# Optimization experiments

Hardware: AMD Instinct MI355X
Metric: run time of the kernel (lower is better)

The kernel has to match this reference:

```python
import jax, jax.numpy as jnp
import numpy as np

B, N = 256, 256
EPS = 1e-5

def _bn_per_sample(x, g, b):
    # Torch code applies BatchNorm1d(C) to each sample (N, C) independently in
    # training mode -> normalize over the node axis per channel, per sample.
    m = jnp.mean(x, axis=1, keepdims=True)
    v = jnp.mean((x - m) ** 2, axis=1, keepdims=True)  # biased var, as BN uses
    return (x - m) * jax.lax.rsqrt(v + EPS) * g + b

def _mpl(adj, x, W):
    # message passing: aggregate over dense adjacency then project + ReLU
    agg = jnp.einsum('nm,bmd->bnd', adj, x)
    return jnp.maximum(agg @ W, 0.0)

def _green(adj, x, W):
    # GreenBlock: concat input with MPL output -> doubles channel dim
    return jnp.concatenate([x, _mpl(adj, x, W)], axis=-1)

def setup_inputs() -> dict:
    key = jax.random.key(0)
    ks = jax.random.split(key, 16)
    def w(k, shape):
        fan_in = shape[0]
        return jax.random.normal(k, shape, jnp.float32) / np.sqrt(fan_in)
    return {
        'x': jax.random.normal(ks[0], (B, N, 1), jnp.float32),
        'adj': jax.random.uniform(ks[1], (N, N), jnp.float32),
        'W_fst': w(ks[2], (1, 64)),
        'W_snd': w(ks[3], (64, 64)),
        'W_thrd': w(ks[4], (128, 128)),
        'W_thrdb': w(ks[5], (256, 256)),
        'W_frth': w(ks[6], (256, 256)),
        'W_ffth': w(ks[7], (320, 256)),
        'bn6_g': jnp.ones((256,), jnp.float32), 'bn6_b': jnp.zeros((256,), jnp.float32),
        'W_svth': w(ks[8], (256, 256)),
        'bn8_g': jnp.ones((512,), jnp.float32), 'bn8_b': jnp.zeros((512,), jnp.float32),
        'W_nnth': w(ks[9], (512, 512)),
        'W_tnth': w(ks[10], (1024, 1024)),
        'W_lvnth': w(ks[11], (1280, 256)),
        'bn12_g': jnp.ones((256,), jnp.float32), 'bn12_b': jnp.zeros((256,), jnp.float32),
        'W_ff1': w(ks[12], (576, 128)), 'b_ff1': jnp.zeros((128,), jnp.float32),
        'W_ff2': w(ks[13], (128, 1)), 'b_ff2': jnp.zeros((1,), jnp.float32),
        'W_final': w(ks[14], (1, 1)),
    }

def reference(x, adj, W_fst, W_snd, W_thrd, W_thrdb, W_frth, W_ffth,
              bn6_g, bn6_b, W_svth, bn8_g, bn8_b, W_nnth, W_tnth, W_lvnth,
              bn12_g, bn12_b, W_ff1, b_ff1, W_ff2, b_ff2, W_final):
    b, n = x.shape[0], x.shape[1]
    skip_1 = x @ W_fst                                   # (B,N,64)
    skip_2 = _green(adj, skip_1, W_snd)                  # (B,N,128)
    skip_2 = _green(adj, skip_2, W_thrd)                 # (B,N,256)
    skip_2 = _mpl(adj, skip_2, W_thrdb)                  # (B,N,256)
    skip_2 = _mpl(adj, skip_2, W_frth)                   # (B,N,256)
    skip_2 = jnp.concatenate([skip_1, skip_2], axis=2)   # (B,N,320)
    skip_2 = skip_2 @ W_ffth                             # (B,N,256)
    skip_2 = _bn_per_sample(skip_2, bn6_g, bn6_b)
    skip_3 = _green(adj, skip_2, W_svth)                 # (B,N,512)
    skip_3 = _bn_per_sample(skip_3, bn8_g, bn8_b)
    skip_3 = _green(adj, skip_3, W_nnth)                 # (B,N,1024)
    skip_3 = _mpl(adj, skip_3, W_tnth)                   # (B,N,1024)
    skip_3 = jnp.concatenate([skip_3, skip_2], axis=2)   # (B,N,1280)
    skip_3 = skip_3 @ W_lvnth                            # (B,N,256)
    skip_3 = _bn_per_sample(skip_3, bn12_g, bn12_b)
    last = jnp.concatenate([skip_3, skip_2, skip_1], axis=2)  # (B,N,576)
    last = jnp.maximum(last @ W_ff1 + b_ff1, 0.0) @ W_ff2 + b_ff2  # (B,N,1)
    last = (last @ W_final).reshape(b, n)
    return jax.nn.softmax(last, axis=-1)
```

## Files before the change

### kernel.cpp

```cpp
#include <hip/hip_runtime.h>
#include <math.h>

#define NBATCH 256
#define NNODE 256
#define FCLAMP 60000.0f

typedef float f32x4 __attribute__((ext_vector_type(4)));
typedef _Float16 half_t;
typedef half_t f16x8 __attribute__((ext_vector_type(8)));
typedef half_t f16x4 __attribute__((ext_vector_type(4)));

__device__ __forceinline__ void split2(float v, half_t& h, half_t& l)
{
    v = fminf(fmaxf(v, -FCLAMP), FCLAMP);
    half_t hh = (half_t)v;
    h = hh;
    l = (half_t)(v - (float)hh);
}

template<bool RELU, bool ACC>
__global__ __launch_bounds__(256)
void gemm_wk2(int M, int N, int K,
              const float* __restrict__ A, int lda,
              const half_t* __restrict__ Bh, const half_t* __restrict__ Bl, int ldb,
              float* __restrict__ C, int ldc,
              const float* __restrict__ bias)
{
    __shared__ half_t Ash[128][40], Asl[128][40];
    __shared__ half_t Bsh[128][40], Bsl[128][40];

    const int nwg  = gridDim.x * gridDim.y;
    const int orig = blockIdx.y * gridDim.x + blockIdx.x;
    const int q = nwg >> 3, r8 = nwg & 7;
    const int xcd = orig & 7, pos = orig >> 3;
    const int wgid = (xcd < r8 ? xcd * (q + 1) : r8 * (q + 1) + (xcd - r8) * q) + pos;
    const int bx = wgid % gridDim.x;
    const int by = wgid / gridDim.x;

    const int tid  = threadIdx.x;
    const int tn0  = bx * 128;
    const int tm0  = by * 128;
    const int lane = tid & 63;
    const int w    = tid >> 6;
    const int wr   = (w >> 1) * 64, wc = (w & 1) * 64;
    const int lr   = lane & 15, ko = lane >> 4;

    const int srow = tid >> 1;
    const int skh  = (tid & 1) * 16;

    f32x4 acc[4][4];
#pragma unroll
    for (int i = 0; i < 4; ++i)
#pragma unroll
        for (int j = 0; j < 4; ++j) acc[i][j] = (f32x4){0.f, 0.f, 0.f, 0.f};

    const float*  aP  = A  + (size_t)(tm0 + srow) * lda + skh;
    const half_t* bhP = Bh + (size_t)(tn0 + srow) * ldb + skh;
    const half_t* blP = Bl + (size_t)(tn0 + srow) * ldb + skh;

    float4 ra0, ra1, ra2, ra3;
    f16x8  rbh0, rbh1, rbl0, rbl1;
    {
        const float4* ap = (const float4*)aP;
        ra0 = ap[0]; ra1 = ap[1]; ra2 = ap[2]; ra3 = ap[3];
        const f16x8* ph = (const f16x8*)bhP;
        const f16x8* pl = (const f16x8*)blP;
        rbh0 = ph[0]; rbh1 = ph[1]; rbl0 = pl[0]; rbl1 = pl[1];
    }

    for (int kb = 0; kb < K; kb += 32) {
        {
            float vv[16] = {ra0.x, ra0.y, ra0.z, ra0.w, ra1.x, ra1.y, ra1.z, ra1.w,
                            ra2.x, ra2.y, ra2.z, ra2.w, ra3.x, ra3.y, ra3.z, ra3.w};
            half_t th[16], tl[16];
#pragma unroll
            for (int j = 0; j < 16; ++j)
                split2(vv[j], th[j], tl[j]);
            *(f16x8*)&Ash[srow][skh]     = *(f16x8*)&th[0];
            *(f16x8*)&Ash[srow][skh + 8] = *(f16x8*)&th[8];
            *(f16x8*)&Asl[srow][skh]     = *(f16x8*)&tl[0];
            *(f16x8*)&Asl[srow][skh + 8] = *(f16x8*)&tl[8];
            *(f16x8*)&Bsh[srow][skh]     = rbh0;
            *(f16x8*)&Bsh[srow][skh + 8] = rbh1;
            *(f16x8*)&Bsl[srow][skh]     = rbl0;
            *(f16x8*)&Bsl[srow][skh + 8] = rbl1;
        }
        __syncthreads();

        if (kb + 32 < K) {
            const float4* ap = (const float4*)(aP + kb + 32);
            ra0 = ap[0]; ra1 = ap[1]; ra2 = ap[2]; ra3 = ap[3];
            const f16x8* ph = (const f16x8*)(bhP + kb + 32);
            const f16x8* pl = (const f16x8*)(blP + kb + 32);
            rbh0 = ph[0]; rbh1 = ph[1]; rbl0 = pl[0]; rbl1 = pl[1];
        }

        f16x8 ah[4], al[4], bh[4], bl[4];
#pragma unroll
        for (int mf = 0; mf < 4; ++mf) {
            int r = wr + mf * 16 + lr;
            ah[mf] = *(const f16x8*)&Ash[r][ko * 8];
            al[mf] = *(const f16x8*)&Asl[r][ko * 8];
        }
#pragma unroll
        for (int nf = 0; nf < 4; ++nf) {
            int c = wc + nf * 16 + lr;
            bh[nf] = *(const f16x8*)&Bsh[c][ko * 8];
            bl[nf] = *(const f16x8*)&Bsl[c][ko * 8];
        }
#pragma unroll
        for (int nf = 0; nf < 4; ++nf) {
#pragma unroll
            for (int mf = 0; mf < 4; ++mf) {
                acc[mf][nf] = __builtin_amdgcn_mfma_f32_16x16x32_f16(ah[mf], bh[nf], acc[mf][nf], 0, 0, 0);
                acc[mf][nf] = __builtin_amdgcn_mfma_f32_16x16x32_f16(ah[mf], bl[nf], acc[mf][nf], 0, 0, 0);
                acc[mf][nf] = __builtin_amdgcn_mfma_f32_16x16x32_f16(al[mf], bh[nf], acc[mf][nf], 0, 0, 0);
            }
        }
        __syncthreads();
    }

#pragma unroll
    for (int mf = 0; mf < 4; ++mf) {
        int r0 = tm0 + wr + mf * 16 + ko * 4;
#pragma unroll
        for (int nf = 0; nf < 4; ++nf) {
            int c = tn0 + wc + nf * 16 + lr;
            float bsv = bias ? bias[c] : 0.f;
#pragma unroll
            for (int r = 0; r < 4; ++r) {
                float* cp = C + (size_t)(r0 + r) * ldc + c;
                float t = acc[mf][nf][r] + bsv;
                if (ACC) t += *cp;
                if (RELU) t = fmaxf(t, 0.f);
                *cp = t;
            }
        }
    }
}

__global__ __launch_bounds__(256)
void gemm_ak2(int K, int ldxt,
              const half_t* __restrict__ Ah, const half_t* __restrict__ Al,
              const half_t* __restrict__ XTh, const half_t* __restrict__ XTl,
              float* __restrict__ C, int ldc, long long sC)
{
    const int z = blockIdx.z;
    C += sC * z;
    const int zoff = z * NNODE;
    const int tid  = threadIdx.x;
    const int tn0  = blockIdx.x * 128;
    const int tm0  = blockIdx.y * 128;
    const int lane = tid & 63;
    const int w    = tid >> 6;
    const int wr   = (w >> 1) * 64, wc = (w & 1) * 64;
    const int lr   = lane & 15, ko = lane >> 4;

    f32x4 acc[4][4];
#pragma unroll
    for (int i = 0; i < 4; ++i)
#pragma unroll
        for (int j = 0; j < 4; ++j) acc[i][j] = (f32x4){0.f, 0.f, 0.f, 0.f};

    size_t aoff[4], boff[4];
#pragma unroll
    for (int mf = 0; mf < 4; ++mf)
        aoff[mf] = (size_t)(tm0 + wr + mf * 16 + lr) * NNODE + ko * 8;
#pragma unroll
    for (int nf = 0; nf < 4; ++nf)
        boff[nf] = (size_t)(tn0 + wc + nf * 16 + lr) * ldxt + zoff + ko * 8;

    for (int kb = 0; kb < K; kb += 32) {
        f16x8 ah[4], al[4];
#pragma unroll
        for (int mf = 0; mf < 4; ++mf) {
            ah[mf] = *(const f16x8*)(Ah + aoff[mf] + kb);
            al[mf] = *(const f16x8*)(Al + aoff[mf] + kb);
        }
#pragma unroll
        for (int nf = 0; nf < 4; ++nf) {
            f16x8 bh = *(const f16x8*)(XTh + boff[nf] + kb);
            f16x8 bl = *(const f16x8*)(XTl + boff[nf] + kb);
#pragma unroll
            for (int mf = 0; mf < 4; ++mf) {
                acc[mf][nf] = __builtin_amdgcn_mfma_f32_16x16x32_f16(ah[mf], bh, acc[mf][nf], 0, 0, 0);
                acc[mf][nf] = __builtin_amdgcn_mfma_f32_16x16x32_f16(ah[mf], bl, acc[mf][nf], 0, 0, 0);
                acc[mf][nf] = __builtin_amdgcn_mfma_f32_16x16x32_f16(al[mf], bh, acc[mf][nf], 0, 0, 0);
            }
        }
    }

#pragma unroll
    for (int mf = 0; mf < 4; ++mf) {
        int r0 = tm0 + wr + mf * 16 + ko * 4;
#pragma unroll
        for (int nf = 0; nf < 4; ++nf) {
            int c = tn0 + wc + nf * 16 + lr;
#pragma unroll
            for (int r = 0; r < 4; ++r)
                C[(size_t)(r0 + r) * ldc + c] = acc[mf][nf][r];
        }
    }
}

__global__ __launch_bounds__(256)
void xpose2_k(const float* __restrict__ X, int ld, int Mtot,
              half_t* __restrict__ Th, half_t* __restrict__ Tl)
{
    __shared__ float tile[32][33];
    const int m0 = blockIdx.x * 32, c0 = blockIdx.y * 32;
    const int t = threadIdx.x;
    {
        int r = t >> 3, cc = (t & 7) * 4;
        float4 v = *(const float4*)(X + (size_t)(m0 + r) * ld + c0 + cc);
        tile[r][cc + 0] = v.x; tile[r][cc + 1] = v.y;
        tile[r][cc + 2] = v.z; tile[r][cc + 3] = v.w;
    }
    __syncthreads();
    {
        int cr = t >> 3, mc = (t & 7) * 4;
        f16x4 h, l;
#pragma unroll
        for (int j = 0; j < 4; ++j) {
            half_t hh, ll;
            split2(tile[mc + j][cr], hh, ll);
            h[j] = hh; l[j] = ll;
        }
        size_t o = (size_t)(c0 + cr) * Mtot + m0 + mc;
        *(f16x4*)(Th + o) = h;
        *(f16x4*)(Tl + o) = l;
    }
}

__global__ __launch_bounds__(256)
void wsplit2_k(const float* __restrict__ W, int K, int N,
               half_t* __restrict__ Th, half_t* __restrict__ Tl)
{
    __shared__ float tile[32][33];
    const int k0 = blockIdx.x * 32, n0 = blockIdx.y * 32;
    const int t = threadIdx.x;
    {
        int kr = t >> 3, nc = (t & 7) * 4;
        float4 v = *(const float4*)(W + (size_t)(k0 + kr) * N + n0 + nc);
        tile[kr][nc + 0] = v.x; tile[kr][nc + 1] = v.y;
        tile[kr][nc + 2] = v.z; tile[kr][nc + 3] = v.w;
    }
    __syncthreads();
    {
        int nr = t >> 3, kc = (t & 7) * 4;
        f16x4 h, l;
#pragma unroll
        for (int j = 0; j < 4; ++j) {
            half_t hh, ll;
            split2(tile[kc + j][nr], hh, ll);
            h[j] = hh; l[j] = ll;
        }
        size_t o = (size_t)(n0 + nr) * K + k0 + kc;
        *(f16x4*)(Th + o) = h;
        *(f16x4*)(Tl + o) = l;
    }
}

__global__ void asplit2_k(const float* __restrict__ A,
                          half_t* __restrict__ Ah, half_t* __restrict__ Al, int n)
{
    int i = blockIdx.x * blockDim.x + threadIdx.x;
    if (i < n) {
        half_t h, l;
        split2(A[i], h, l);
        Ah[i] = h; Al[i] = l;
    }
}

template<bool RELU, bool ACC>
__global__ __launch_bounds__(256)
void gemm_k(int M, int N, int K,
            const float* __restrict__ A, int lda, long long sA,
            const float* __restrict__ B, int ldb, long long sB,
            float* __restrict__ C, int ldc, long long sC)
{
    constexpr int BM = 128, BN_ = 64, BK = 16, TM = 8, TN = 4;
    constexpr int TX = BN_ / TN;
    __shared__ float As[BK][BM + 4];
    __shared__ float Bs[BK][BN_ + 4];
    const int bz = blockIdx.z;
    A += sA * bz; B += sB * bz; C += sC * bz;
    const int tn0 = blockIdx.x * BN_, tm0 = blockIdx.y * BM;
    const int tid = threadIdx.x;
    const int tx = tid % TX, ty = tid / TX;
    float acc[TM][TN];
#pragma unroll
    for (int i = 0; i < TM; ++i)
#pragma unroll
        for (int j = 0; j < TN; ++j) acc[i][j] = 0.f;
    const int arow = tid >> 2, akq = tid & 3;
    const int bcq = tid % 16, bkr = tid / 16;
    for (int k0 = 0; k0 < K; k0 += BK) {
#pragma unroll
        for (int i = 0; i < 2; ++i) {
            int row = arow + i * 64;
            float4 a = *(const float4*)(A + (size_t)(tm0 + row) * lda + k0 + akq * 4);
            As[akq * 4 + 0][row] = a.x; As[akq * 4 + 1][row] = a.y;
            As[akq * 4 + 2][row] = a.z; As[akq * 4 + 3][row] = a.w;
        }
        {
            float4 b4 = *(const float4*)(B + (size_t)(k0 + bkr) * ldb + tn0 + bcq * 4);
            *(float4*)&Bs[bkr][bcq * 4] = b4;
        }
        __syncthreads();
#pragma unroll
        for (int k = 0; k < BK; ++k) {
            float av[TM], bv[TN];
#pragma unroll
            for (int i = 0; i < TM; ++i) av[i] = As[k][ty * TM + i];
#pragma unroll
            for (int j = 0; j < TN; ++j) bv[j] = Bs[k][tx * TN + j];
#pragma unroll
            for (int i = 0; i < TM; ++i)
#pragma unroll
                for (int j = 0; j < TN; ++j)
                    acc[i][j] = fmaf(av[i], bv[j], acc[i][j]);
        }
        __syncthreads();
    }
#pragma unroll
    for (int i = 0; i < TM; ++i) {
        size_t r = (size_t)tm0 + ty * TM + i;
        int c = tn0 + tx * TN;
        float t0 = acc[i][0], t1 = acc[i][1], t2 = acc[i][2], t3 = acc[i][3];
        float* cp = C + r * ldc + c;
        if (ACC) {
            float4 p = *(const float4*)cp;
            t0 += p.x; t1 += p.y; t2 += p.z; t3 += p.w;
        }
        if (RELU) {
            t0 = fmaxf(t0, 0.f); t1 = fmaxf(t1, 0.f);
            t2 = fmaxf(t2, 0.f); t3 = fmaxf(t3, 0.f);
        }
        float4 v; v.x = t0; v.y = t1; v.z = t2; v.w = t3;
        *(float4*)cp = v;
    }
}

__global__ void s1_k(const float* __restrict__ x, const float* __restrict__ Wfst,
                     float* __restrict__ dst)
{
    int idx = blockIdx.x * blockDim.x + threadIdx.x;
    int r = idx >> 4, c4 = idx & 15;
    float xv = x[r];
    float4 wv = *(const float4*)(Wfst + c4 * 4);
    float4 o; o.x = xv * wv.x; o.y = xv * wv.y; o.z = xv * wv.z; o.w = xv * wv.w;
    *(float4*)(dst + (size_t)r * 576 + c4 * 4) = o;
}

__global__ __launch_bounds__(256)
void bn_k(const float* __restrict__ src, int lds_, float* __restrict__ dst, int ldd,
          const float* __restrict__ g, const float* __restrict__ bt)
{
    const int b = blockIdx.x, c0 = blockIdx.y * 64;
    const int cl = threadIdx.x & 63, ph = threadIdx.x >> 6;
    const int c = c0 + cl;
    const float* Sb = src + (size_t)b * NNODE * lds_;
    float* Db = dst + (size_t)b * NNODE * ldd;
    double sum = 0.0, sq = 0.0;
    for (int n = ph; n < NNODE; n += 4) {
        double v = (double)Sb[(size_t)n * lds_ + c];
        sum += v; sq += v * v;
    }
    __shared__ double ssum[4][64], ssq[4][64];
    __shared__ float sscale[64], sshift[64];
    ssum[ph][cl] = sum; ssq[ph][cl] = sq;
    __syncthreads();
    if (ph == 0) {
        double s = ssum[0][cl] + ssum[1][cl] + ssum[2][cl] + ssum[3][cl];
        double q = ssq[0][cl] + ssq[1][cl] + ssq[2][cl] + ssq[3][cl];
        double m = s * (1.0 / NNODE);
        double var = q * (1.0 / NNODE) - m * m;
        double sc = (double)g[c] / sqrt(var + 1e-5);
        sscale[cl] = (float)sc;
        sshift[cl] = (float)((double)bt[c] - m * sc);
    }
    __syncthreads();
    float sc = sscale[cl], sh = sshift[cl];
    for (int n = ph; n < NNODE; n += 4)
        Db[(size_t)n * ldd + c] = fmaf(Sb[(size_t)n * lds_ + c], sc, sh);
}

__global__ __launch_bounds__(256)
void head_k(const float* __restrict__ H, const float* __restrict__ Wff2,
            const float* __restrict__ bff2, const float* __restrict__ Wfin,
            float* __restrict__ out)
{
    __shared__ float wsm[128];
    __shared__ float red[256];
    const int b = blockIdx.x, n = threadIdx.x;
    if (n < 128) wsm[n] = Wff2[n];
    __syncthreads();
    const float* h = H + ((size_t)b * NNODE + n) * 128;
    float dot = 0.f;
#pragma unroll
    for (int k = 0; k < 128; k += 4) {
        float4 hv = *(const float4*)(h + k);
        dot = fmaf(hv.x, wsm[k + 0], dot); dot = fmaf(hv.y, wsm[k + 1], dot);
        dot = fmaf(hv.z, wsm[k + 2], dot); dot = fmaf(hv.w, wsm[k + 3], dot);
    }
    float logit = (dot + bff2[0]) * Wfin[0];
    red[n] = logit; __syncthreads();
    for (int s = 128; s > 0; s >>= 1) {
        if (n < s) red[n] = fmaxf(red[n], red[n + s]);
        __syncthreads();
    }
    float mx = red[0]; __syncthreads();
    float e = expf(logit - mx);
    red[n] = e; __syncthreads();
    for (int s = 128; s > 0; s >>= 1) {
        if (n < s) red[n] += red[n + s];
        __syncthreads();
    }
    out[(size_t)b * NNODE + n] = e / red[0];
}

__global__ void zero_k(float* p, int n)
{
    int i = blockIdx.x * blockDim.x + threadIdx.x;
    if (i < n) p[i] = 0.f;
}

static inline void g(bool relu, bool acc, int M, int N, int K,
    const float* A, int lda, long long sA,
    const float* B, int ldb, long long sB,
    float* C, int ldc, long long sC, int nb, hipStream_t s)
{
    dim3 grid(N / 64, M / 128, nb), blk(256);
    if ( relu &&  acc) gemm_k<true,  true ><<<grid, blk, 0, s>>>(M,N,K,A,lda,sA,B,ldb,sB,C,ldc,sC);
    if ( relu && !acc) gemm_k<true,  false><<<grid, blk, 0, s>>>(M,N,K,A,lda,sA,B,ldb,sB,C,ldc,sC);
    if (!relu &&  acc) gemm_k<false, true ><<<grid, blk, 0, s>>>(M,N,K,A,lda,sA,B,ldb,sB,C,ldc,sC);
    if (!relu && !acc) gemm_k<false, false><<<grid, blk, 0, s>>>(M,N,K,A,lda,sA,B,ldb,sB,C,ldc,sC);
}

static inline void wk2(bool relu, bool acc, int M, int N, int K,
                       const float* A, int lda,
                       const half_t* Bh, const half_t* Bl, int ldb,
                       float* C, int ldc, const float* bias, hipStream_t s)
{
    dim3 grid(N / 128, M / 128, 1), blk(256);
    if (relu  &&  acc) gemm_wk2<true,  true ><<<grid, blk, 0, s>>>(M, N, K, A, lda, Bh, Bl, ldb, C, ldc, bias);
    if (relu  && !acc) gemm_wk2<true,  false><<<grid, blk, 0, s>>>(M, N, K, A, lda, Bh, Bl, ldb, C, ldc, bias);
    if (!relu &&  acc) gemm_wk2<false, true ><<<grid, blk, 0, s>>>(M, N, K, A, lda, Bh, Bl, ldb, C, ldc, bias);
    if (!relu && !acc) gemm_wk2<false, false><<<grid, blk, 0, s>>>(M, N, K, A, lda, Bh, Bl, ldb, C, ldc, bias);
}

struct Ctx {
    const half_t *ajh, *ajl;
    half_t *XT;
    int RSc, nb;
    hipStream_t s;
};

static inline void ak2(const Ctx& cx, int Cch, const float* X, int ldx,
                       float* Cout, int ldc, long long sC)
{
    half_t* X0 = cx.XT;
    half_t* X1 = X0 + (size_t)Cch * cx.RSc;
    xpose2_k<<<dim3(cx.RSc / 32, Cch / 32), 256, 0, cx.s>>>(X, ldx, cx.RSc, X0, X1);
    gemm_ak2<<<dim3(Cch / 128, 2, cx.nb), 256, 0, cx.s>>>(NNODE, cx.RSc,
        cx.ajh, cx.ajl, X0, X1, Cout, ldc, sC);
}

struct Weights {
    const float *adj, *W_fst, *W_snd, *W_thrd, *W_thrdb, *W_frth, *W_ffth;
    const float *bn6_g, *bn6_b, *W_svth, *bn8_g, *bn8_b, *W_nnth, *W_tnth;
    const float *W_lvnth, *bn12_g, *bn12_b, *W_ff1, *b_ff1, *W_ff2, *b_ff2, *W_final;
};
struct WT2 { half_t *h, *l; };

static void run_chunk(const float* x, float* out, float* ws, int nb,
                      const Weights& W, const WT2* V, const Ctx& cx0,
                      hipStream_t stream)
{
    const int RSc = nb * NNODE;
    const size_t CH = (size_t)RSc;
    float* SS = ws;
    float* S3 = SS;
    float* S2 = SS + 256;
    float* S1 = SS + 512;
    float* U  = ws + 576 * CH;
    float* Q0 = U;
    float* Q1 = U + 256 * CH;
    float* Q2 = U + 512 * CH;
    float* Q3 = U + 768 * CH;
    float* R  = ws + 1600 * CH;
    float* R512 = ws + 1600 * CH;
    half_t* XTb = (half_t*)(ws + 2112 * CH);

    Ctx cx = cx0; cx.XT = XTb; cx.RSc = RSc; cx.nb = nb; cx.s = stream;
    const float* adj = W.adj;
    const long long SN = (long long)NNODE;
    const long long S576 = SN * 576, S256 = SN * 256, S1024 = SN * 1024,
                    S128 = SN * 128, S64 = SN * 64;

    s1_k<<<RSc / 16, 256, 0, stream>>>(x, W.W_fst, S1);
    g(0,0, NNODE,64,NNODE, adj,NNODE,0, S1,576,S576, Q0,256,S256, nb, stream);
    g(1,0, RSc,64,64, Q0,256,0, W.W_snd,64,0, Q1,64,0, 1, stream);
    g(0,0, NNODE,64,NNODE, adj,NNODE,0, Q1,64,S64, Q0+64,256,S256, nb, stream);
    g(1,0, RSc,128,128, Q0,256,0, W.W_thrd,128,0, Q2,128,0, 1, stream);
    g(0,0, NNODE,128,NNODE, adj,NNODE,0, Q2,128,S128, Q0+128,256,S256, nb, stream);
    g(1,0, RSc,256,256, Q0,256,0, W.W_thrdb,256,0, Q1,256,0, 1, stream);
    g(0,0, NNODE,256,NNODE, adj,NNODE,0, Q1,256,S256, Q2,256,S256, nb, stream);
    g(1,0, RSc,256,256, Q2,256,0, W.W_frth,256,0, Q3,256,0, 1, stream);
    g(0,0, RSc,256,64,  S1,576,0, W.W_ffth,          256,0, S2,576,0, 1, stream);
    g(0,1, RSc,256,256, Q3,256,0, W.W_ffth + 64*256, 256,0, S2,576,0, 1, stream);
    bn_k<<<dim3(nb, 4), 256, 0, stream>>>(S2, 576, S2, 576, W.bn6_g, W.bn6_b);

    ak2(cx, 256, S2, 576, R, 256, S256);
    wk2(1, 0, RSc, 256, 256, R, 256, V[0].h, V[0].l, 256, U + 512, 1024, 0, stream);
    bn_k<<<dim3(nb, 4), 256, 0, stream>>>(S2, 576, R, 256, W.bn8_g, W.bn8_b);
    bn_k<<<dim3(nb, 4), 256, 0, stream>>>(U + 512, 1024, U + 512, 1024,
                                          W.bn8_g + 256, W.bn8_b + 256);
    ak2(cx, 256, R, 256, U, 1024, S1024);
    ak2(cx, 256, U + 512, 1024, U + 256, 1024, S1024);
    wk2(1, 0, RSc, 512, 512, U, 1024, V[1].h, V[1].l, 512, R512, 512, 0, stream);
    ak2(cx, 256, R512,       512, U + 512, 1024, S1024);
    ak2(cx, 256, R512 + 256, 512, U + 768, 1024, S1024);
    for (int h = 0; h < 2; ++h) {
        wk2(1, 0, RSc, 512, 1024, U, 1024,
            V[2].h + (size_t)h * 512 * 1024, V[2].l + (size_t)h * 512 * 1024, 1024,
            R512, 512, 0, stream);
        wk2(0, h > 0, RSc, 256, 512, R512, 512,
            V[3].h + (size_t)h * 512, V[3].l + (size_t)h * 512, 1280,
            S3, 576, 0, stream);
    }
    wk2(0, 1, RSc, 256, 256, S2, 576,
        V[3].h + 1024, V[3].l + 1024, 1280, S3, 576, 0, stream);
    bn_k<<<dim3(nb, 4), 256, 0, stream>>>(S3, 576, S3, 576, W.bn12_g, W.bn12_b);
    wk2(1, 0, RSc, 128, 576, SS, 576, V[4].h, V[4].l, 576, U, 128, W.b_ff1, stream);
    head_k<<<nb, 256, 0, stream>>>(U, W.W_ff2, W.b_ff2, W.W_final, out);
}

extern "C" void kernel_launch(void* const* d_in, const int* in_sizes, int n_in,
                              void* d_out, int out_size, void* d_ws, size_t ws_size,
                              hipStream_t stream)
{
    const float* x = (const float*)d_in[0];
    Weights W;
    W.adj = (const float*)d_in[1];   W.W_fst  = (const float*)d_in[2];
    W.W_snd = (const float*)d_in[3]; W.W_thrd = (const float*)d_in[4];
    W.W_thrdb = (const float*)d_in[5]; W.W_frth = (const float*)d_in[6];
    W.W_ffth = (const float*)d_in[7]; W.bn6_g = (const float*)d_in[8];
    W.bn6_b = (const float*)d_in[9];  W.W_svth = (const float*)d_in[10];
    W.bn8_g = (const float*)d_in[11]; W.bn8_b = (const float*)d_in[12];
    W.W_nnth = (const float*)d_in[13]; W.W_tnth = (const float*)d_in[14];
    W.W_lvnth = (const float*)d_in[15]; W.bn12_g = (const float*)d_in[16];
    W.bn12_b = (const float*)d_in[17]; W.W_ff1 = (const float*)d_in[18];
    W.b_ff1 = (const float*)d_in[19]; W.W_ff2 = (const float*)d_in[20];
    W.b_ff2 = (const float*)d_in[21]; W.W_final = (const float*)d_in[22];
    float* out = (float*)d_out;

    const size_t szs[5] = {65536, 262144, 1048576, 327680, 73728};
    const size_t ADJSZ = 65536;
    size_t tot_halves = 2 * ADJSZ;
    for (int i = 0; i < 5; ++i) tot_halves += 2 * szs[i];
    const size_t split_bytes = tot_halves * 2;

    int nb = NBATCH;
    while (nb > 0 && (size_t)2368 * nb * NNODE * 4 + split_bytes > ws_size) nb -= 32;
    if (nb <= 0) {
        zero_k<<<(out_size + 255) / 256, 256, 0, stream>>>(out, out_size);
        return;
    }

    float* ws = (float*)d_ws;
    half_t* hb = (half_t*)(ws + (size_t)2368 * nb * NNODE);
    WT2 V[5];
    size_t off = 0;
    for (int i = 0; i < 5; ++i) {
        V[i].h = hb + off; off += szs[i];
        V[i].l = hb + off; off += szs[i];
    }
    half_t* ajh = hb + off; off += ADJSZ;
    half_t* ajl = hb + off; off += ADJSZ;

    const float* wp[5] = {W.W_svth, W.W_nnth, W.W_tnth, W.W_lvnth, W.W_ff1};
    const int wkk[5] = {256, 512, 1024, 1280, 576};
    const int wnn[5] = {256, 512, 1024, 256, 128};
    for (int i = 0; i < 5; ++i)
        wsplit2_k<<<dim3(wkk[i] / 32, wnn[i] / 32), 256, 0, stream>>>(
            wp[i], wkk[i], wnn[i], V[i].h, V[i].l);
    asplit2_k<<<256, 256, 0, stream>>>(W.adj, ajh, ajl, 65536);

    Ctx cx0; cx0.ajh = ajh; cx0.ajl = ajl;
    cx0.XT = nullptr; cx0.RSc = 0; cx0.nb = 0; cx0.s = stream;

    for (int b0 = 0; b0 < NBATCH; b0 += nb) {
        int nbc = (NBATCH - b0 < nb) ? (NBATCH - b0) : nb;
        run_chunk(x + (size_t)b0 * NNODE, out + (size_t)b0 * NNODE,
                  ws, nbc, W, V, cx0, stream);
    }
}
```

Before: 2.863 ms.

## Fuse activation transpose and fp16 split into adjacency GEMM via LDS staging

Removes the separate transpose-and-split kernel that wrote fp16 hi/lo transposed copies of activations to global memory. The adjacency GEMM now reads fp32 activations directly, splits them into hi/lo halves and stages them in shared memory each K-step, with barriers around the tile. This saves a global round trip and a launch per aggregation and frees workspace so larger batch chunks fit, at the cost of redundant split work across M-tiles and added syncs without double buffering.

```diff
diff --git a/kernel.cpp b/kernel.cpp
--- a/kernel.cpp
+++ b/kernel.cpp
@@ -140,14 +140,15 @@
 }
 
 __global__ __launch_bounds__(256)
-void gemm_ak2(int K, int ldxt,
-              const half_t* __restrict__ Ah, const half_t* __restrict__ Al,
-              const half_t* __restrict__ XTh, const half_t* __restrict__ XTl,
-              float* __restrict__ C, int ldc, long long sC)
-{
+void gemm_ak2f(int K, const half_t* __restrict__ Ah, const half_t* __restrict__ Al,
+               const float* __restrict__ X, int ldx,
+               float* __restrict__ C, int ldc, long long sC)
+{
+    __shared__ half_t Bsh[128][40], Bsl[128][40];
+
     const int z = blockIdx.z;
     C += sC * z;
-    const int zoff = z * NNODE;
+    const long long zoff = (long long)z * NNODE;
     const int tid  = threadIdx.x;
     const int tn0  = blockIdx.x * 128;
     const int tm0  = blockIdx.y * 128;
@@ -156,38 +157,62 @@
     const int wr   = (w >> 1) * 64, wc = (w & 1) * 64;
     const int lr   = lane & 15, ko = lane >> 4;
 
+    const int sc  = tid & 127;
+    const int skh = (tid >> 7) * 16;
+
     f32x4 acc[4][4];
 #pragma unroll
     for (int i = 0; i < 4; ++i)
 #pragma unroll
         for (int j = 0; j < 4; ++j) acc[i][j] = (f32x4){0.f, 0.f, 0.f, 0.f};
 
-    size_t aoff[4], boff[4];
+    size_t aoff[4];
 #pragma unroll
     for (int mf = 0; mf < 4; ++mf)
         aoff[mf] = (size_t)(tm0 + wr + mf * 16 + lr) * NNODE + ko * 8;
-#pragma unroll
-    for (int nf = 0; nf < 4; ++nf)
-        boff[nf] = (size_t)(tn0 + wc + nf * 16 + lr) * ldxt + zoff + ko * 8;
+
+    const float* xP = X + (size_t)(zoff + skh) * ldx + tn0 + sc;
 
     for (int kb = 0; kb < K; kb += 32) {
+        {
+            float v[16];
+#pragma unroll
+            for (int i = 0; i < 16; ++i)
+                v[i] = xP[(size_t)(kb + i) * ldx];
+            half_t th[16], tl[16];
+#pragma unroll
+            for (int i = 0; i < 16; ++i)
+                split2(v[i], th[i], tl[i]);
+            *(f16x8*)&Bsh[sc][skh]     = *(f16x8*)&th[0];
+            *(f16x8*)&Bsh[sc][skh + 8] = *(f16x8*)&th[8];
+            *(f16x8*)&Bsl[sc][skh]     = *(f16x8*)&tl[0];
+            *(f16x8*)&Bsl[sc][skh + 8] = *(f16x8*)&tl[8];
+        }
+        __syncthreads();
+
         f16x8 ah[4], al[4];
 #pragma unroll
         for (int mf = 0; mf < 4; ++mf) {
             ah[mf] = *(const f16x8*)(Ah + aoff[mf] + kb);
             al[mf] = *(const f16x8*)(Al + aoff[mf] + kb);
         }
+        f16x8 bh[4], bl[4];
 #pragma unroll
         for (int nf = 0; nf < 4; ++nf) {
-            f16x8 bh = *(const f16x8*)(XTh + boff[nf] + kb);
-            f16x8 bl = *(const f16x8*)(XTl + boff[nf] + kb);
+            int c = wc + nf * 16 + lr;
+            bh[nf] = *(const f16x8*)&Bsh[c][ko * 8];
+            bl[nf] = *(const f16x8*)&Bsl[c][ko * 8];
+        }
+#pragma unroll
+        for (int nf = 0; nf < 4; ++nf) {
 #pragma unroll
             for (int mf = 0; mf < 4; ++mf) {
-                acc[mf][nf] = __builtin_amdgcn_mfma_f32_16x16x32_f16(ah[mf], bh, acc[mf][nf], 0, 0, 0);
-                acc[mf][nf] = __builtin_amdgcn_mfma_f32_16x16x32_f16(ah[mf], bl, acc[mf][nf], 0, 0, 0);
-                acc[mf][nf] = __builtin_amdgcn_mfma_f32_16x16x32_f16(al[mf], bh, acc[mf][nf], 0, 0, 0);
+                acc[mf][nf] = __builtin_amdgcn_mfma_f32_16x16x32_f16(ah[mf], bh[nf], acc[mf][nf], 0, 0, 0);
+                acc[mf][nf] = __builtin_amdgcn_mfma_f32_16x16x32_f16(ah[mf], bl[nf], acc[mf][nf], 0, 0, 0);
+                acc[mf][nf] = __builtin_amdgcn_mfma_f32_16x16x32_f16(al[mf], bh[nf], acc[mf][nf], 0, 0, 0);
             }
         }
+        __syncthreads();
     }
 
 #pragma unroll
@@ -200,35 +225,6 @@
             for (int r = 0; r < 4; ++r)
                 C[(size_t)(r0 + r) * ldc + c] = acc[mf][nf][r];
         }
-    }
-}
-
-__global__ __launch_bounds__(256)
-void xpose2_k(const float* __restrict__ X, int ld, int Mtot,
-              half_t* __restrict__ Th, half_t* __restrict__ Tl)
-{
-    __shared__ float tile[32][33];
-    const int m0 = blockIdx.x * 32, c0 = blockIdx.y * 32;
-    const int t = threadIdx.x;
-    {
-        int r = t >> 3, cc = (t & 7) * 4;
-        float4 v = *(const float4*)(X + (size_t)(m0 + r) * ld + c0 + cc);
-        tile[r][cc + 0] = v.x; tile[r][cc + 1] = v.y;
-        tile[r][cc + 2] = v.z; tile[r][cc + 3] = v.w;
-    }
-    __syncthreads();
-    {
-        int cr = t >> 3, mc = (t & 7) * 4;
-        f16x4 h, l;
-#pragma unroll
-        for (int j = 0; j < 4; ++j) {
-            half_t hh, ll;
-            split2(tile[mc + j][cr], hh, ll);
-            h[j] = hh; l[j] = ll;
-        }
-        size_t o = (size_t)(c0 + cr) * Mtot + m0 + mc;
-        *(f16x4*)(Th + o) = h;
-        *(f16x4*)(Tl + o) = l;
     }
 }
 
@@ -452,19 +448,15 @@
 
 struct Ctx {
     const half_t *ajh, *ajl;
-    half_t *XT;
-    int RSc, nb;
+    int nb;
     hipStream_t s;
 };
 
 static inline void ak2(const Ctx& cx, int Cch, const float* X, int ldx,
                        float* Cout, int ldc, long long sC)
 {
-    half_t* X0 = cx.XT;
-    half_t* X1 = X0 + (size_t)Cch * cx.RSc;
-    xpose2_k<<<dim3(cx.RSc / 32, Cch / 32), 256, 0, cx.s>>>(X, ldx, cx.RSc, X0, X1);
-    gemm_ak2<<<dim3(Cch / 128, 2, cx.nb), 256, 0, cx.s>>>(NNODE, cx.RSc,
-        cx.ajh, cx.ajl, X0, X1, Cout, ldc, sC);
+    gemm_ak2f<<<dim3(Cch / 128, NNODE / 128, cx.nb), 256, 0, cx.s>>>(
+        NNODE, cx.ajh, cx.ajl, X, ldx, Cout, ldc, sC);
 }
 
 struct Weights {
@@ -491,9 +483,8 @@
     float* Q3 = U + 768 * CH;
     float* R  = ws + 1600 * CH;
     float* R512 = ws + 1600 * CH;
-    half_t* XTb = (half_t*)(ws + 2112 * CH);
-
-    Ctx cx = cx0; cx.XT = XTb; cx.RSc = RSc; cx.nb = nb; cx.s = stream;
+
+    Ctx cx = cx0; cx.nb = nb; cx.s = stream;
     const float* adj = W.adj;
     const long long SN = (long long)NNODE;
     const long long S576 = SN * 576, S256 = SN * 256, S1024 = SN * 1024,
@@ -563,14 +554,14 @@
     const size_t split_bytes = tot_halves * 2;
 
     int nb = NBATCH;
-    while (nb > 0 && (size_t)2368 * nb * NNODE * 4 + split_bytes > ws_size) nb -= 32;
+    while (nb > 0 && (size_t)2112 * nb * NNODE * 4 + split_bytes > ws_size) nb -= 32;
     if (nb <= 0) {
         zero_k<<<(out_size + 255) / 256, 256, 0, stream>>>(out, out_size);
         return;
     }
 
     float* ws = (float*)d_ws;
-    half_t* hb = (half_t*)(ws + (size_t)2368 * nb * NNODE);
+    half_t* hb = (half_t*)(ws + (size_t)2112 * nb * NNODE);
     WT2 V[5];
     size_t off = 0;
     for (int i = 0; i < 5; ++i) {
@@ -588,8 +579,7 @@
             wp[i], wkk[i], wnn[i], V[i].h, V[i].l);
     asplit2_k<<<256, 256, 0, stream>>>(W.adj, ajh, ajl, 65536);
 
-    Ctx cx0; cx0.ajh = ajh; cx0.ajl = ajl;
-    cx0.XT = nullptr; cx0.RSc = 0; cx0.nb = 0; cx0.s = stream;
+    Ctx cx0; cx0.ajh = ajh; cx0.ajl = ajl; cx0.nb = 0; cx0.s = stream;
 
     for (int b0 = 0; b0 < NBATCH; b0 += nb) {
         int nbc = (NBATCH - b0 < nb) ? (NBATCH - b0) : nb;
```

After: 2.640 ms. -7.8%, faster.
